# Optimization experiments

Hardware: AMD Instinct MI355X
Metric: run time of the kernel (lower is better)

Reference implementation:

```python
import jax, jax.numpy as jnp
import numpy as np

N_USERS = 100000
N_ITEMS = 200000
N_NODES = N_USERS + N_ITEMS
EMB = 64
N_HOPS = 3
NNZ = 2000000
EDGE_RATE = 0.5   # edge_dropout_rate
MESS_RATE = 0.1   # mess_dropout_rate


def setup_inputs() -> dict:
    key = jax.random.key(0)
    k1, k2, k3, k4, k5 = jax.random.split(key, 5)
    user_embed = jax.random.normal(k1, (N_USERS, EMB), dtype=jnp.float32) * 0.1
    item_embed = jax.random.normal(k2, (N_ITEMS, EMB), dtype=jnp.float32) * 0.1
    adj_rows = jax.random.randint(k3, (NNZ,), 0, N_NODES, dtype=jnp.int32)
    adj_cols = jax.random.randint(k4, (NNZ,), 0, N_NODES, dtype=jnp.int32)
    # normalized adjacency values (positive, small) like D^-1/2 A D^-1/2 entries
    adj_vals = jax.random.uniform(k5, (NNZ,), dtype=jnp.float32) * 0.1
    return {
        "user_embed": user_embed,
        "item_embed": item_embed,
        "adj_vals": adj_vals,
        "adj_rows": adj_rows,
        "adj_cols": adj_cols,
    }


def reference(user_embed, item_embed, adj_vals, adj_rows, adj_cols):
    # all_embed: [N_NODES, EMB]
    agg = jnp.concatenate([user_embed, item_embed], axis=0)
    drop_key = jax.random.key(42)
    embs = []
    for hop in range(N_HOPS):
        ekey = jax.random.fold_in(drop_key, 2 * hop)
        mkey = jax.random.fold_in(drop_key, 2 * hop + 1)
        # sparse edge dropout: mask = floor(rate + U[0,1)) -> keep w.p. rate,
        # rescale kept values by 1/(1-rate), exactly as _sparse_dropout
        edge_keep = jnp.floor(EDGE_RATE + jax.random.uniform(ekey, (NNZ,))) > 0
        v = jnp.where(edge_keep, adj_vals, 0.0) * (1.0 / (1.0 - EDGE_RATE))
        # SpMM: out[r] += v_e * agg[c] for each edge e=(r,c)
        msgs = v[:, None] * agg[adj_cols]                 # [NNZ, EMB]
        agg = jax.ops.segment_sum(msgs, adj_rows, num_segments=N_NODES)
        # message dropout (nn.Dropout): keep w.p. 1-p, scale 1/(1-p)
        keep = jax.random.uniform(mkey, agg.shape) >= MESS_RATE
        agg = jnp.where(keep, agg, 0.0) * (1.0 / (1.0 - MESS_RATE))
        embs.append(agg)
    embs = jnp.stack(embs, axis=1)  # [N_NODES, N_HOPS, EMB]
    # original returns (embs[:n_users], embs[n_users:]); we return the
    # concatenated stack (identical math, split is a view)
    return embs
```

## Files before the change

### kernel.cpp

```cpp
#include <hip/hip_runtime.h>
#include <cstdint>

static constexpr int kUsers  = 100000;
static constexpr int kItems  = 200000;
static constexpr int kNodes  = 300000;
static constexpr int kEmb    = 64;
static constexpr int kHops   = 3;
static constexpr int kNnz    = 2000000;
static constexpr int kStride = kHops * kEmb;

#define MESS_SCALE ((float)(1.0 / 0.9))

__host__ __device__ inline void tf2x32(uint32_t k0, uint32_t k1, uint32_t& x0, uint32_t& x1) {
  uint32_t k2 = k0 ^ k1 ^ 0x1BD11BDAu;
  x0 += k0; x1 += k1;
#define TFR(r) { x0 += x1; x1 = (x1 << (r)) | (x1 >> (32 - (r))); x1 ^= x0; }
  TFR(13) TFR(15) TFR(26) TFR(6)
  x0 += k1; x1 += k2 + 1u;
  TFR(17) TFR(29) TFR(16) TFR(24)
  x0 += k2; x1 += k0 + 2u;
  TFR(13) TFR(15) TFR(26) TFR(6)
  x0 += k0; x1 += k1 + 3u;
  TFR(17) TFR(29) TFR(16) TFR(24)
  x0 += k1; x1 += k2 + 4u;
  TFR(13) TFR(15) TFR(26) TFR(6)
  x0 += k2; x1 += k0 + 5u;
#undef TFR
}

__device__ inline uint32_t draw_bits(uint32_t k0, uint32_t k1, uint32_t i) {
  uint32_t x0 = 0u, x1 = i;
  tf2x32(k0, k1, x0, x1);
  return x0 ^ x1;
}

__device__ inline float bits_to_unit(uint32_t bits) {
  return __uint_as_float((bits >> 9) | 0x3F800000u) - 1.0f;
}


__global__ void hist_k(const int* __restrict__ rows, int* __restrict__ deg) {
  int e = blockIdx.x * blockDim.x + threadIdx.x;
  if (e < kNnz) atomicAdd(&deg[rows[e]], 1);
}

__global__ void alloc_k(const int* __restrict__ deg, int* __restrict__ start,
                        int* __restrict__ cur, int* __restrict__ cursor) {
  int r = blockIdx.x * blockDim.x + threadIdx.x;
  int lane = threadIdx.x & 63;
  int d = (r < kNodes) ? deg[r] : 0;
  int x = d;
  for (int off = 1; off < 64; off <<= 1) {
    int y = __shfl_up(x, off);
    if (lane >= off) x += y;
  }
  int excl = x - d;
  int total = __shfl(x, 63);
  int base = 0;
  if (lane == 63) base = atomicAdd(cursor, total);
  base = __shfl(base, 63);
  if (r < kNodes) { start[r] = base + excl; cur[r] = base + excl; }
}

__global__ void fill_k(const int* __restrict__ rows, const int* __restrict__ cols,
                       const float* __restrict__ vals, int* __restrict__ cur,
                       int4* __restrict__ pv) {
  int e = blockIdx.x * blockDim.x + threadIdx.x;
  if (e >= kNnz) return;
  int r = rows[e];
  int p = atomicAdd(&cur[r], 1);
  pv[p] = make_int4(cols[e], e, __float_as_int(vals[e]), 0);
}


__global__ void edge_vals_csr_k(int4* __restrict__ pv, uint32_t ek0, uint32_t ek1) {
  int p = blockIdx.x * blockDim.x + threadIdx.x;
  if (p >= kNnz) return;
  int4 ee = pv[p];
  uint32_t bits = draw_bits(ek0, ek1, (uint32_t)ee.y);
  float v = (bits & 0x80000000u) ? __int_as_float(ee.z) * 2.0f : 0.0f;
  ((int*)pv)[4 * p + 3] = __float_as_int(v);
}

template <bool HOP0>
__global__ void row_gather_k(const int* __restrict__ start, const int* __restrict__ endp,
                             const int4* __restrict__ pv,
                             const float* __restrict__ ue, const float* __restrict__ ie,
                             const float* __restrict__ prev,
                             float* __restrict__ out, uint32_t mk0, uint32_t mk1, int hop) {
  int wid = (int)(((long long)blockIdx.x * blockDim.x + threadIdx.x) >> 6);
  int d = threadIdx.x & 63;
  if (wid >= kNodes) return;
  int s = endp ? start[wid] : 0;
  int e = endp[wid];
  float acc = 0.0f;
  const float* isft = ie - (long long)kUsers * kEmb;
  for (int k = s; k < e; k += 4) {
    int i1 = (k + 1 < e) ? k + 1 : e - 1;
    int i2 = (k + 2 < e) ? k + 2 : e - 1;
    int i3 = (k + 3 < e) ? k + 3 : e - 1;
    int4 e0 = pv[k], e1 = pv[i1], e2 = pv[i2], e3 = pv[i3];
    float v0 = __int_as_float(e0.w);
    float v1 = (k + 1 < e) ? __int_as_float(e1.w) : 0.0f;
    float v2 = (k + 2 < e) ? __int_as_float(e2.w) : 0.0f;
    float v3 = (k + 3 < e) ? __int_as_float(e3.w) : 0.0f;
    float x0, x1, x2, x3;
    if (HOP0) {
      const float* b0 = (e0.x < kUsers) ? ue : isft;
      const float* b1 = (e1.x < kUsers) ? ue : isft;
      const float* b2 = (e2.x < kUsers) ? ue : isft;
      const float* b3 = (e3.x < kUsers) ? ue : isft;
      x0 = b0[(long long)e0.x * kEmb + d];
      x1 = b1[(long long)e1.x * kEmb + d];
      x2 = b2[(long long)e2.x * kEmb + d];
      x3 = b3[(long long)e3.x * kEmb + d];
    } else {
      x0 = prev[(long long)e0.x * kStride + d];
      x1 = prev[(long long)e1.x * kStride + d];
      x2 = prev[(long long)e2.x * kStride + d];
      x3 = prev[(long long)e3.x * kStride + d];
    }
    acc += v0 * x0 + v1 * x1 + v2 * x2 + v3 * x3;
  }
  uint32_t bits = draw_bits(mk0, mk1, (uint32_t)(wid * kEmb + d));
  float u = bits_to_unit(bits);
  float res = (u >= 0.1f) ? acc * MESS_SCALE : 0.0f;
  out[(long long)wid * kStride + hop * kEmb + d] = res;
}


__global__ void edge_vals_k(const float* __restrict__ adj_vals, float* __restrict__ v_out,
                            uint32_t ek0, uint32_t ek1) {
  int e = blockIdx.x * blockDim.x + threadIdx.x;
  if (e >= kNnz) return;
  uint32_t bits = draw_bits(ek0, ek1, (uint32_t)e);
  v_out[e] = (bits & 0x80000000u) ? adj_vals[e] * 2.0f : 0.0f;
}

__global__ void scatter_k(const int* __restrict__ rows, const int* __restrict__ cols,
                          const float* __restrict__ vvals,
                          const float* __restrict__ user_emb, const float* __restrict__ item_emb,
                          const float* __restrict__ prev, float* __restrict__ acc) {
  long long t = (long long)blockIdx.x * blockDim.x + threadIdx.x;
  int e = (int)(t >> 6);
  int d = (int)(t & 63);
  if (e >= kNnz) return;
  float ve = vvals[e];
  if (ve == 0.0f) return;
  int c = cols[e];
  int r = rows[e];
  float x;
  if (prev) x = prev[(long long)c * kStride + d];
  else x = (c < kUsers) ? user_emb[(long long)c * kEmb + d]
                        : item_emb[(long long)(c - kUsers) * kEmb + d];
  unsafeAtomicAdd(&acc[(long long)r * kStride + d], ve * x);
}

__global__ void mess_k(float* __restrict__ slice, uint32_t mk0, uint32_t mk1) {
  long long i = (long long)blockIdx.x * blockDim.x + threadIdx.x;
  const long long total = (long long)kNodes * kEmb;
  if (i >= total) return;
  uint32_t bits = draw_bits(mk0, mk1, (uint32_t)i);
  float u = bits_to_unit(bits);
  int n = (int)(i >> 6), d = (int)(i & 63);
  long long idx = (long long)n * kStride + d;
  float val = slice[idx];
  slice[idx] = (u >= 0.1f) ? val * MESS_SCALE : 0.0f;
}


extern "C" void kernel_launch(void* const* d_in, const int* in_sizes, int n_in,
                              void* d_out, int out_size, void* d_ws, size_t ws_size,
                              hipStream_t stream) {
  const float* user_emb = (const float*)d_in[0];
  const float* item_emb = (const float*)d_in[1];
  const float* adj_vals = (const float*)d_in[2];
  const int*   adj_rows = (const int*)d_in[3];
  const int*   adj_cols = (const int*)d_in[4];
  float* out = (float*)d_out;

  char* base = (char*)d_ws;
  const size_t off_deg    = 0;
  const size_t off_start  = 1200128;
  const size_t off_cur    = 2400256;
  const size_t off_cursor = 3600384;
  const size_t off_pv     = 3600896;
  const size_t needed     = 35600896;

  uint32_t ek0[kHops], ek1[kHops], mk0[kHops], mk1[kHops];
  for (int hop = 0; hop < kHops; ++hop) {
    ek0[hop] = 0u; ek1[hop] = (uint32_t)(2 * hop);
    tf2x32(0u, 42u, ek0[hop], ek1[hop]);
    mk0[hop] = 0u; mk1[hop] = (uint32_t)(2 * hop + 1);
    tf2x32(0u, 42u, mk0[hop], mk1[hop]);
  }

  if (ws_size >= needed) {
    int*  deg    = (int*)(base + off_deg);
    int*  start  = (int*)(base + off_start);
    int*  cur    = (int*)(base + off_cur);
    int*  cursor = (int*)(base + off_cursor);
    int4* pv     = (int4*)(base + off_pv);

    hipMemsetAsync(deg, 0, (size_t)kNodes * sizeof(int), stream);
    hipMemsetAsync(cursor, 0, sizeof(int), stream);

    hist_k<<<(kNnz + 255) / 256, 256, 0, stream>>>(adj_rows, deg);
    alloc_k<<<(kNodes + 255) / 256, 256, 0, stream>>>(deg, start, cur, cursor);
    fill_k<<<(kNnz + 255) / 256, 256, 0, stream>>>(adj_rows, adj_cols, adj_vals, cur, pv);

    long long nthreads = (long long)kNodes * 64;
    int ngrid = (int)((nthreads + 255) / 256);
    for (int hop = 0; hop < kHops; ++hop) {
      edge_vals_csr_k<<<(kNnz + 255) / 256, 256, 0, stream>>>(pv, ek0[hop], ek1[hop]);
      if (hop == 0) {
        row_gather_k<true><<<ngrid, 256, 0, stream>>>(
            start, cur, pv, user_emb, item_emb, nullptr, out, mk0[hop], mk1[hop], hop);
      } else {
        const float* prev = out + (long long)(hop - 1) * kEmb;
        row_gather_k<false><<<ngrid, 256, 0, stream>>>(
            start, cur, pv, user_emb, item_emb, prev, out, mk0[hop], mk1[hop], hop);
      }
    }
  } else {
    float* vbuf = (float*)d_ws;
    hipMemsetAsync(d_out, 0, (size_t)out_size * sizeof(float), stream);
    for (int hop = 0; hop < kHops; ++hop) {
      edge_vals_k<<<(kNnz + 255) / 256, 256, 0, stream>>>(adj_vals, vbuf, ek0[hop], ek1[hop]);
      const float* prev = (hop == 0) ? nullptr : (out + (long long)(hop - 1) * kEmb);
      float* acc = out + (long long)hop * kEmb;
      long long nthreads = (long long)kNnz * 64;
      scatter_k<<<(int)((nthreads + 255) / 256), 256, 0, stream>>>(
          adj_rows, adj_cols, vbuf, user_emb, item_emb, prev, acc);
      long long etotal = (long long)kNodes * kEmb;
      mess_k<<<(int)((etotal + 255) / 256), 256, 0, stream>>>(acc, mk0[hop], mk1[hop]);
    }
  }
}
```

Baseline: 974.2 us.

## Build CSR via two-level bucket sort and unroll gather with dropped-edge reuse

Replaces the per-row atomic histogram, scan and fill with a two-level sort. Edges are first binned into 64-row buckets split into 8 sub-bins to spread atomic contention, then each bucket is sorted by row in shared memory, which keeps record writes local. The gather loop is unrolled to 8 edges and loads only the col/value half of each record. Dropped edges are redirected to a single shared column so their embedding loads hit cache. The single-block scan kernel and the fixed shared-memory capacity per bucket add serial work and assume bucket sizes stay bounded.

```diff
diff --git a/kernel.cpp b/kernel.cpp
--- a/kernel.cpp
+++ b/kernel.cpp
@@ -8,6 +8,10 @@
 static constexpr int kHops   = 3;
 static constexpr int kNnz    = 2000000;
 static constexpr int kStride = kHops * kEmb;
+
+static constexpr int kBShift   = 6;
+static constexpr int kNBuckets = (kNodes + 63) >> kBShift;
+static constexpr int kNB8      = kNBuckets * 8;
 
 #define MESS_SCALE ((float)(1.0 / 0.9))
 
@@ -39,88 +43,163 @@
 }
 
 
-__global__ void hist_k(const int* __restrict__ rows, int* __restrict__ deg) {
-  int e = blockIdx.x * blockDim.x + threadIdx.x;
-  if (e < kNnz) atomicAdd(&deg[rows[e]], 1);
-}
-
-__global__ void alloc_k(const int* __restrict__ deg, int* __restrict__ start,
-                        int* __restrict__ cur, int* __restrict__ cursor) {
-  int r = blockIdx.x * blockDim.x + threadIdx.x;
-  int lane = threadIdx.x & 63;
-  int d = (r < kNodes) ? deg[r] : 0;
-  int x = d;
-  for (int off = 1; off < 64; off <<= 1) {
-    int y = __shfl_up(x, off);
-    if (lane >= off) x += y;
-  }
-  int excl = x - d;
-  int total = __shfl(x, 63);
-  int base = 0;
-  if (lane == 63) base = atomicAdd(cursor, total);
-  base = __shfl(base, 63);
-  if (r < kNodes) { start[r] = base + excl; cur[r] = base + excl; }
-}
-
-__global__ void fill_k(const int* __restrict__ rows, const int* __restrict__ cols,
-                       const float* __restrict__ vals, int* __restrict__ cur,
-                       int4* __restrict__ pv) {
+__global__ void hist2_k(const int* __restrict__ rows, int* __restrict__ cnt) {
   int e = blockIdx.x * blockDim.x + threadIdx.x;
   if (e >= kNnz) return;
+  int grp = blockIdx.x & 7;
+  atomicAdd(&cnt[((rows[e] >> kBShift) << 3) + grp], 1);
+}
+
+__global__ void scan_k(const int* __restrict__ cnt, int* __restrict__ sub_base,
+                       int* __restrict__ bucketbase, int* __restrict__ start) {
+  __shared__ int wsum[4];
+  __shared__ int carry_s;
+  int tid = threadIdx.x;
+  int lane = tid & 63, wv = tid >> 6;
+  if (tid == 0) carry_s = 0;
+  __syncthreads();
+  for (int base = 0; base < kNB8; base += 256) {
+    int i = base + tid;
+    int v = (i < kNB8) ? cnt[i] : 0;
+    int x = v;
+    for (int off = 1; off < 64; off <<= 1) {
+      int y = __shfl_up(x, off);
+      if (lane >= off) x += y;
+    }
+    if (lane == 63) wsum[wv] = x;
+    __syncthreads();
+    int woff = 0;
+    if (wv >= 1) woff += wsum[0];
+    if (wv >= 2) woff += wsum[1];
+    if (wv >= 3) woff += wsum[2];
+    int excl = carry_s + woff + (x - v);
+    if (i < kNB8) sub_base[i] = excl;
+    __syncthreads();
+    if (tid == 0) carry_s += wsum[0] + wsum[1] + wsum[2] + wsum[3];
+    __syncthreads();
+  }
+  for (int b = tid; b < kNBuckets; b += 256) bucketbase[b] = sub_base[b << 3];
+  if (tid == 0) { bucketbase[kNBuckets] = kNnz; start[kNodes] = kNnz; }
+}
+
+__global__ void phase1_k(const int* __restrict__ rows, const int* __restrict__ cols,
+                         const float* __restrict__ vals,
+                         const int* __restrict__ sub_base, int* __restrict__ bcur,
+                         int4* __restrict__ pv) {
+  int e = blockIdx.x * blockDim.x + threadIdx.x;
+  if (e >= kNnz) return;
+  int grp = blockIdx.x & 7;
   int r = rows[e];
-  int p = atomicAdd(&cur[r], 1);
-  pv[p] = make_int4(cols[e], e, __float_as_int(vals[e]), 0);
+  int slot = ((r >> kBShift) << 3) + grp;
+  int p = sub_base[slot] + atomicAdd(&bcur[slot], 1);
+  pv[p] = make_int4(e, __float_as_int(vals[e]), cols[e], r);
+}
+
+__global__ void phase2_k(const int* __restrict__ bucketbase, int4* __restrict__ pv,
+                         int* __restrict__ start) {
+  constexpr int LCAP = 2048;
+  constexpr int RPT  = 8;
+  __shared__ int4 sbuf[LCAP];
+  __shared__ int rcnt[64];
+  __shared__ int rcur[64];
+  int tid = threadIdx.x;
+  int b = blockIdx.x;
+  int base = bucketbase[b], end = bucketbase[b + 1];
+  int n = end - base;
+  int r0 = b << kBShift;
+  if (tid < 64) rcnt[tid] = 0;
+  __syncthreads();
+  int4 rreg[RPT];
+  for (int i = tid; i < n && i < LCAP; i += 256) {
+    int4 rec = pv[base + i];
+    sbuf[i] = rec;
+    atomicAdd(&rcnt[rec.w - r0], 1);
+  }
+#pragma unroll
+  for (int j = 0; j < RPT; ++j) {
+    int i = LCAP + j * 256 + tid;
+    if (i < n) {
+      int4 rec = pv[base + i];
+      rreg[j] = rec;
+      atomicAdd(&rcnt[rec.w - r0], 1);
+    }
+  }
+  __syncthreads();
+  if (tid < 64) {
+    int v = rcnt[tid];
+    int x = v;
+    for (int off = 1; off < 64; off <<= 1) {
+      int y = __shfl_up(x, off);
+      if (tid >= off) x += y;
+    }
+    int excl = x - v;
+    rcur[tid] = base + excl;
+    int r = r0 + tid;
+    if (r < kNodes) start[r] = base + excl;
+  }
+  __syncthreads();
+  for (int i = tid; i < n && i < LCAP; i += 256) {
+    int4 rec = sbuf[i];
+    int dst = atomicAdd(&rcur[rec.w - r0], 1);
+    pv[dst] = rec;
+  }
+#pragma unroll
+  for (int j = 0; j < RPT; ++j) {
+    int i = LCAP + j * 256 + tid;
+    if (i < n) {
+      int4 rec = rreg[j];
+      int dst = atomicAdd(&rcur[rec.w - r0], 1);
+      pv[dst] = rec;
+    }
+  }
 }
 
 
 __global__ void edge_vals_csr_k(int4* __restrict__ pv, uint32_t ek0, uint32_t ek1) {
   int p = blockIdx.x * blockDim.x + threadIdx.x;
   if (p >= kNnz) return;
-  int4 ee = pv[p];
-  uint32_t bits = draw_bits(ek0, ek1, (uint32_t)ee.y);
-  float v = (bits & 0x80000000u) ? __int_as_float(ee.z) * 2.0f : 0.0f;
+  int2 ev = ((const int2*)pv)[2 * p];
+  uint32_t bits = draw_bits(ek0, ek1, (uint32_t)ev.x);
+  float v = (bits & 0x80000000u) ? __int_as_float(ev.y) * 2.0f : 0.0f;
   ((int*)pv)[4 * p + 3] = __float_as_int(v);
 }
 
 template <bool HOP0>
-__global__ void row_gather_k(const int* __restrict__ start, const int* __restrict__ endp,
-                             const int4* __restrict__ pv,
-                             const float* __restrict__ ue, const float* __restrict__ ie,
-                             const float* __restrict__ prev,
-                             float* __restrict__ out, uint32_t mk0, uint32_t mk1, int hop) {
+__global__ __launch_bounds__(256, 4) void row_gather_k(
+    const int* __restrict__ start, const int* __restrict__ endp,
+    const int4* __restrict__ pv,
+    const float* __restrict__ ue, const float* __restrict__ ie,
+    const float* __restrict__ prev,
+    float* __restrict__ out, uint32_t mk0, uint32_t mk1, int hop) {
   int wid = (int)(((long long)blockIdx.x * blockDim.x + threadIdx.x) >> 6);
   int d = threadIdx.x & 63;
   if (wid >= kNodes) return;
-  int s = endp ? start[wid] : 0;
+  int s = start[wid];
   int e = endp[wid];
   float acc = 0.0f;
   const float* isft = ie - (long long)kUsers * kEmb;
-  for (int k = s; k < e; k += 4) {
-    int i1 = (k + 1 < e) ? k + 1 : e - 1;
-    int i2 = (k + 2 < e) ? k + 2 : e - 1;
-    int i3 = (k + 3 < e) ? k + 3 : e - 1;
-    int4 e0 = pv[k], e1 = pv[i1], e2 = pv[i2], e3 = pv[i3];
-    float v0 = __int_as_float(e0.w);
-    float v1 = (k + 1 < e) ? __int_as_float(e1.w) : 0.0f;
-    float v2 = (k + 2 < e) ? __int_as_float(e2.w) : 0.0f;
-    float v3 = (k + 3 < e) ? __int_as_float(e3.w) : 0.0f;
-    float x0, x1, x2, x3;
-    if (HOP0) {
-      const float* b0 = (e0.x < kUsers) ? ue : isft;
-      const float* b1 = (e1.x < kUsers) ? ue : isft;
-      const float* b2 = (e2.x < kUsers) ? ue : isft;
-      const float* b3 = (e3.x < kUsers) ? ue : isft;
-      x0 = b0[(long long)e0.x * kEmb + d];
-      x1 = b1[(long long)e1.x * kEmb + d];
-      x2 = b2[(long long)e2.x * kEmb + d];
-      x3 = b3[(long long)e3.x * kEmb + d];
-    } else {
-      x0 = prev[(long long)e0.x * kStride + d];
-      x1 = prev[(long long)e1.x * kStride + d];
-      x2 = prev[(long long)e2.x * kStride + d];
-      x3 = prev[(long long)e3.x * kStride + d];
-    }
-    acc += v0 * x0 + v1 * x1 + v2 * x2 + v3 * x3;
+  const int2* pvh = (const int2*)pv;
+  if (e > s) {
+    int c0 = pvh[2 * s + 1].x;
+    for (int k = s; k < e; k += 8) {
+#pragma unroll
+      for (int j = 0; j < 8; ++j) {
+        int kk = k + j;
+        bool live = kk < e;
+        int idx = live ? kk : s;
+        int2 cv = pvh[2 * idx + 1];
+        float v = live ? __int_as_float(cv.y) : 0.0f;
+        int c = (v != 0.0f) ? cv.x : c0;
+        float x;
+        if (HOP0) {
+          const float* bp = (c < kUsers) ? ue : isft;
+          x = bp[(long long)c * kEmb + d];
+        } else {
+          x = prev[(long long)c * kStride + d];
+        }
+        acc += v * x;
+      }
+    }
   }
   uint32_t bits = draw_bits(mk0, mk1, (uint32_t)(wid * kEmb + d));
   float u = bits_to_unit(bits);
@@ -180,12 +259,13 @@
   float* out = (float*)d_out;
 
   char* base = (char*)d_ws;
-  const size_t off_deg    = 0;
-  const size_t off_start  = 1200128;
-  const size_t off_cur    = 2400256;
-  const size_t off_cursor = 3600384;
-  const size_t off_pv     = 3600896;
-  const size_t needed     = 35600896;
+  const size_t off_start = 0;
+  const size_t off_cnt   = 1200128;
+  const size_t off_sub   = 1350144;
+  const size_t off_bcur  = 1500160;
+  const size_t off_bbase = 1650176;
+  const size_t off_pv    = 1669120;
+  const size_t needed    = 33669120;
 
   uint32_t ek0[kHops], ek1[kHops], mk0[kHops], mk1[kHops];
   for (int hop = 0; hop < kHops; ++hop) {
@@ -196,30 +276,33 @@
   }
 
   if (ws_size >= needed) {
-    int*  deg    = (int*)(base + off_deg);
-    int*  start  = (int*)(base + off_start);
-    int*  cur    = (int*)(base + off_cur);
-    int*  cursor = (int*)(base + off_cursor);
-    int4* pv     = (int4*)(base + off_pv);
-
-    hipMemsetAsync(deg, 0, (size_t)kNodes * sizeof(int), stream);
-    hipMemsetAsync(cursor, 0, sizeof(int), stream);
-
-    hist_k<<<(kNnz + 255) / 256, 256, 0, stream>>>(adj_rows, deg);
-    alloc_k<<<(kNodes + 255) / 256, 256, 0, stream>>>(deg, start, cur, cursor);
-    fill_k<<<(kNnz + 255) / 256, 256, 0, stream>>>(adj_rows, adj_cols, adj_vals, cur, pv);
+    int*  start = (int*)(base + off_start);
+    int*  cnt   = (int*)(base + off_cnt);
+    int*  subb  = (int*)(base + off_sub);
+    int*  bcur  = (int*)(base + off_bcur);
+    int*  bbase = (int*)(base + off_bbase);
+    int4* pv    = (int4*)(base + off_pv);
+
+    hipMemsetAsync(cnt, 0, (size_t)kNB8 * sizeof(int), stream);
+    hipMemsetAsync(bcur, 0, (size_t)kNB8 * sizeof(int), stream);
+
+    const int egrid = (kNnz + 255) / 256;
+    hist2_k<<<egrid, 256, 0, stream>>>(adj_rows, cnt);
+    scan_k<<<1, 256, 0, stream>>>(cnt, subb, bbase, start);
+    phase1_k<<<egrid, 256, 0, stream>>>(adj_rows, adj_cols, adj_vals, subb, bcur, pv);
+    phase2_k<<<kNBuckets, 256, 0, stream>>>(bbase, pv, start);
 
     long long nthreads = (long long)kNodes * 64;
     int ngrid = (int)((nthreads + 255) / 256);
     for (int hop = 0; hop < kHops; ++hop) {
-      edge_vals_csr_k<<<(kNnz + 255) / 256, 256, 0, stream>>>(pv, ek0[hop], ek1[hop]);
+      edge_vals_csr_k<<<egrid, 256, 0, stream>>>(pv, ek0[hop], ek1[hop]);
       if (hop == 0) {
         row_gather_k<true><<<ngrid, 256, 0, stream>>>(
-            start, cur, pv, user_emb, item_emb, nullptr, out, mk0[hop], mk1[hop], hop);
+            start, start + 1, pv, user_emb, item_emb, nullptr, out, mk0[hop], mk1[hop], hop);
       } else {
         const float* prev = out + (long long)(hop - 1) * kEmb;
         row_gather_k<false><<<ngrid, 256, 0, stream>>>(
-            start, cur, pv, user_emb, item_emb, prev, out, mk0[hop], mk1[hop], hop);
+            start, start + 1, pv, user_emb, item_emb, prev, out, mk0[hop], mk1[hop], hop);
       }
     }
   } else {
```

Measured after the change: 1.239 ms. 27.2% more time.
